# Kernel tuning notes

Hardware: AMD Instinct MI355X
Metric: run time of the kernel (lower is better)

The kernel has to match this reference:

```python
import jax, jax.numpy as jnp
import numpy as np

N_CLASSES = 80
N_ANCHORS = 3
ANCHORS = [[0.02403, 0.03125], [0.05469, 0.08221], [0.12109, 0.15104]]


def setup_inputs() -> dict:
    key = jax.random.key(0)
    B, W, H = 32, 76, 76
    C = (5 + N_CLASSES) * N_ANCHORS  # 255
    inputs = jax.random.normal(key, (B, C, W, H), dtype=jnp.float32)
    # anchors: [3,2] -> swapaxes -> [2,3] -> unsqueeze twice -> [2,1,1,3]
    anchors = jnp.asarray(ANCHORS, dtype=jnp.float32).swapaxes(0, 1).reshape(2, 1, 1, N_ANCHORS)
    return {"inputs": inputs, "anchors": anchors}


def reference(inputs, anchors):
    B, C, W, H = inputs.shape
    # split(85, dim=1) then cat on new last dim == reshape to [B,3,85,W,H] and
    # move the anchor-group axis to the end -> [B, 85, W, H, n_anchors]
    x = inputs.reshape(B, N_ANCHORS, 5 + N_CLASSES, W, H).transpose(0, 2, 3, 4, 1)
    t_xy = x[:, 0:2]            # [B,2,W,H,A]
    t_wh = x[:, 2:4]            # [B,2,W,H,A]
    objectness = x[:, 4:5]      # [B,1,W,H,A]
    class_prob = x[:, 5:]       # [B,80,W,H,A]

    # grid offsets: meshgrid 'ij' -> grid[0][i,j]=i, grid[1][i,j]=j
    gi, gj = jnp.meshgrid(jnp.arange(W), jnp.arange(H), indexing="ij")
    grid = jnp.stack([gi, gj], axis=0).reshape(1, 2, W, H, 1).astype(jnp.float32)
    n = jnp.asarray([W, H], dtype=jnp.float32).reshape(1, 2, 1, 1, 1)

    b_xy = (jax.nn.sigmoid(t_xy) + grid) / n          # [B,2,W,H,A]
    b_wh = jnp.exp(t_wh) * anchors                    # [B,2,W,H,A]

    conf = jax.nn.sigmoid(class_prob) * jax.nn.sigmoid(objectness)  # [B,80,W,H,A]
    conf = conf.reshape(B, N_CLASSES, -1).transpose(0, 2, 1)         # [B, W*H*A, 80]
    scores = jnp.max(conf, axis=2)                                   # [B, W*H*A]

    half = b_wh * 0.5
    x1y1 = b_xy - half
    x2y2 = b_xy + half
    boxes = jnp.concatenate([x1y1, x2y2], axis=1)     # [B,4,W,H,A]
    boxes = boxes.reshape(B, 4, -1).transpose(0, 2, 1)  # [B, W*H*A, 4]
    return boxes, conf, scores
```

## Files before the change

kernel.cpp:

```cpp
#include <hip/hip_runtime.h>


#define NCLS 80
#define NA   3
#define BB   32
#define WW   76
#define HH   76
#define WH   (WW*HH)
#define PP   (WH*NA)
#define TS   152
#define NT   38
#define CROW 84

typedef float f32x4 __attribute__((ext_vector_type(4)));

__global__ __launch_bounds__(512, 6) void yolo_conf_kernel(
    const float* __restrict__ in,
    float* __restrict__ conf,
    float* __restrict__ scores,
    float* __restrict__ scores_ws,
    int use_ws)
{
    __shared__ float cls[TS * CROW];
    __shared__ float so_arr[TS];

    const int t    = threadIdx.x;
    const int bid  = blockIdx.x;
    const int tile = bid % NT;
    const int ba   = bid / NT;
    const int a    = ba % NA;
    const int b    = ba / NA;
    const int s0   = tile * TS;

    const float* aplane = in + ((size_t)b * 255 + a * 85) * WH;

    if (t < TS)
        so_arr[t] = 1.0f / (1.0f + __expf(-aplane[(size_t)4 * WH + s0 + t]));

    #pragma unroll 3
    for (int it = 0; it < 6; ++it) {
        int u = it * 512 + t;
        if (u < 20 * TS) {
            int qq = u / TS;
            int sl = u - qq * TS;
            const float* gp = aplane + (size_t)(5 + qq * 4) * WH + s0 + sl;
            float v0 = gp[0];
            float v1 = gp[(size_t)1 * WH];
            float v2 = gp[(size_t)2 * WH];
            float v3 = gp[(size_t)3 * WH];
            *reinterpret_cast<float4*>(&cls[sl * CROW + qq * 4]) =
                make_float4(v0, v1, v2, v3);
        }
    }

    __syncthreads();

    size_t cbase = ((size_t)b * PP + (size_t)s0 * 3 + a) * NCLS;
    #pragma unroll 3
    for (int it = 0; it < 6; ++it) {
        int q = it * 512 + t;
        if (q < 20 * TS) {
            int sl = q / 20;
            int u  = q - sl * 20;
            float4 tv = *reinterpret_cast<const float4*>(&cls[sl * CROW + u * 4]);
            float so = so_arr[sl];
            f32x4 o;
            o.x = so / (1.0f + __expf(-tv.x));
            o.y = so / (1.0f + __expf(-tv.y));
            o.z = so / (1.0f + __expf(-tv.z));
            o.w = so / (1.0f + __expf(-tv.w));
            __builtin_nontemporal_store(o,
                reinterpret_cast<f32x4*>(conf + cbase + (size_t)sl * 240 + u * 4));
        }
    }

    if (t < TS) {
        float mx = -1e30f;
        #pragma unroll
        for (int u = 0; u < 20; ++u) {
            float4 v = *reinterpret_cast<const float4*>(&cls[t * CROW + u * 4]);
            mx = fmaxf(mx, fmaxf(fmaxf(v.x, v.y), fmaxf(v.z, v.w)));
        }
        float sc = so_arr[t] * (1.0f / (1.0f + __expf(-mx)));
        if (use_ws) {
            __builtin_nontemporal_store(sc,
                scores_ws + ((size_t)b * NA + a) * WH + s0 + t);
        } else {
            scores[(size_t)b * PP + (size_t)(s0 + t) * 3 + a] = sc;
        }
    }
}

__global__ __launch_bounds__(512, 4) void yolo_box_kernel(
    const float* __restrict__ in,
    const float* __restrict__ anchors,
    float* __restrict__ boxes,
    float* __restrict__ scores,
    const float* __restrict__ scores_ws,
    int use_ws)
{
    __shared__ float4 box_buf[TS * NA];
    __shared__ float  sc_buf[TS * NA];

    const int t    = threadIdx.x;
    const int bid  = blockIdx.x;
    const int tile = bid % NT;
    const int b    = bid / NT;
    const int s0   = tile * TS;

    if (t < TS * NA) {
        int aa = t / TS;
        int sl = t - aa * TS;
        int s  = s0 + sl;
        const float* hp = in + ((size_t)b * 255 + aa * 85) * WH + s;
        float tx = hp[0];
        float ty = hp[(size_t)1 * WH];
        float tw = hp[(size_t)2 * WH];
        float th = hp[(size_t)3 * WH];

        int w = s / HH, h = s - w * HH;
        float sx = 1.0f / (1.0f + __expf(-tx));
        float sy = 1.0f / (1.0f + __expf(-ty));
        float bx = (sx + (float)w) * (1.0f / WW);
        float by = (sy + (float)h) * (1.0f / HH);
        float bw = __expf(tw) * anchors[aa];
        float bh = __expf(th) * anchors[3 + aa];

        box_buf[sl * NA + aa] = make_float4(bx - 0.5f * bw, by - 0.5f * bh,
                                            bx + 0.5f * bw, by + 0.5f * bh);
        if (use_ws)
            sc_buf[sl * NA + aa] = scores_ws[((size_t)b * NA + aa) * WH + s];
    }

    __syncthreads();

    if (t < TS * NA) {
        float4 bq = box_buf[t];
        f32x4 bo = {bq.x, bq.y, bq.z, bq.w};
        __builtin_nontemporal_store(bo,
            reinterpret_cast<f32x4*>(boxes + ((size_t)b * PP + s0 * 3 + t) * 4));
        if (use_ws) {
            __builtin_nontemporal_store(sc_buf[t],
                scores + (size_t)b * PP + s0 * 3 + t);
        }
    }
}

extern "C" void kernel_launch(void* const* d_in, const int* in_sizes, int n_in,
                              void* d_out, int out_size, void* d_ws, size_t ws_size,
                              hipStream_t stream) {
    const float* in      = (const float*)d_in[0];
    const float* anchors = (const float*)d_in[1];

    float* boxes  = (float*)d_out;
    float* conf   = boxes + (size_t)BB * PP * 4;
    float* scores = conf + (size_t)BB * PP * NCLS;

    const size_t ws_need = (size_t)BB * NA * WH * sizeof(float);
    int use_ws = ws_size >= ws_need ? 1 : 0;
    float* scores_ws = (float*)d_ws;

    yolo_conf_kernel<<<BB * NA * NT, 512, 0, stream>>>(
        in, conf, scores, scores_ws, use_ws);
    yolo_box_kernel<<<BB * NT, 512, 0, stream>>>(
        in, anchors, boxes, scores, scores_ws, use_ws);
}
```

Measured before the change: 73.28 us.

## Fuse conf and box kernels into one decode kernel with XCD-aware block remap

Merges the two kernels into a single kernel in which each workgroup handles one 76-pixel tile across all three anchors. It computes boxes, objectness and per-anchor class confidences in one pass and writes scores directly, with no scores workspace round-trip. Block indices are remapped so consecutive tiles land on the same XCD, and the tile size is halved. This removes a kernel launch and the workspace traffic, at the cost of an anchor loop with two barriers per anchor and less parallelism per block.

```diff
diff --git a/kernel.cpp b/kernel.cpp
--- a/kernel.cpp
+++ b/kernel.cpp
@@ -8,141 +8,119 @@
 #define HH   76
 #define WH   (WW*HH)
 #define PP   (WH*NA)
-#define TS   152
-#define NT   38
+#define TS   76
+#define NTILE 76
 #define CROW 84
+#define NWG  (BB * NTILE)
+#define CPX  (NWG / 8)
 
 typedef float f32x4 __attribute__((ext_vector_type(4)));
 
-__global__ __launch_bounds__(512, 6) void yolo_conf_kernel(
-    const float* __restrict__ in,
-    float* __restrict__ conf,
-    float* __restrict__ scores,
-    float* __restrict__ scores_ws,
-    int use_ws)
-{
-    __shared__ float cls[TS * CROW];
-    __shared__ float so_arr[TS];
-
-    const int t    = threadIdx.x;
-    const int bid  = blockIdx.x;
-    const int tile = bid % NT;
-    const int ba   = bid / NT;
-    const int a    = ba % NA;
-    const int b    = ba / NA;
-    const int s0   = tile * TS;
-
-    const float* aplane = in + ((size_t)b * 255 + a * 85) * WH;
-
-    if (t < TS)
-        so_arr[t] = 1.0f / (1.0f + __expf(-aplane[(size_t)4 * WH + s0 + t]));
-
-    #pragma unroll 3
-    for (int it = 0; it < 6; ++it) {
-        int u = it * 512 + t;
-        if (u < 20 * TS) {
-            int qq = u / TS;
-            int sl = u - qq * TS;
-            const float* gp = aplane + (size_t)(5 + qq * 4) * WH + s0 + sl;
-            float v0 = gp[0];
-            float v1 = gp[(size_t)1 * WH];
-            float v2 = gp[(size_t)2 * WH];
-            float v3 = gp[(size_t)3 * WH];
-            *reinterpret_cast<float4*>(&cls[sl * CROW + qq * 4]) =
-                make_float4(v0, v1, v2, v3);
-        }
-    }
-
-    __syncthreads();
-
-    size_t cbase = ((size_t)b * PP + (size_t)s0 * 3 + a) * NCLS;
-    #pragma unroll 3
-    for (int it = 0; it < 6; ++it) {
-        int q = it * 512 + t;
-        if (q < 20 * TS) {
-            int sl = q / 20;
-            int u  = q - sl * 20;
-            float4 tv = *reinterpret_cast<const float4*>(&cls[sl * CROW + u * 4]);
-            float so = so_arr[sl];
-            f32x4 o;
-            o.x = so / (1.0f + __expf(-tv.x));
-            o.y = so / (1.0f + __expf(-tv.y));
-            o.z = so / (1.0f + __expf(-tv.z));
-            o.w = so / (1.0f + __expf(-tv.w));
-            __builtin_nontemporal_store(o,
-                reinterpret_cast<f32x4*>(conf + cbase + (size_t)sl * 240 + u * 4));
-        }
-    }
-
-    if (t < TS) {
-        float mx = -1e30f;
-        #pragma unroll
-        for (int u = 0; u < 20; ++u) {
-            float4 v = *reinterpret_cast<const float4*>(&cls[t * CROW + u * 4]);
-            mx = fmaxf(mx, fmaxf(fmaxf(v.x, v.y), fmaxf(v.z, v.w)));
-        }
-        float sc = so_arr[t] * (1.0f / (1.0f + __expf(-mx)));
-        if (use_ws) {
-            __builtin_nontemporal_store(sc,
-                scores_ws + ((size_t)b * NA + a) * WH + s0 + t);
-        } else {
-            scores[(size_t)b * PP + (size_t)(s0 + t) * 3 + a] = sc;
-        }
-    }
-}
-
-__global__ __launch_bounds__(512, 4) void yolo_box_kernel(
+__global__ __launch_bounds__(512, 8) void yolo_decode_kernel(
     const float* __restrict__ in,
     const float* __restrict__ anchors,
     float* __restrict__ boxes,
-    float* __restrict__ scores,
-    const float* __restrict__ scores_ws,
-    int use_ws)
+    float* __restrict__ conf,
+    float* __restrict__ scores)
 {
+    __shared__ float  cls[TS * CROW];
+    __shared__ float  so_buf[TS * NA];
+    __shared__ float  sc_buf[TS * NA];
     __shared__ float4 box_buf[TS * NA];
-    __shared__ float  sc_buf[TS * NA];
 
     const int t    = threadIdx.x;
-    const int bid  = blockIdx.x;
-    const int tile = bid % NT;
-    const int b    = bid / NT;
+    const int hw   = blockIdx.x;
+    const int bid  = (hw & 7) * CPX + (hw >> 3);
+    const int tile = bid % NTILE;
+    const int b    = bid / NTILE;
     const int s0   = tile * TS;
 
+    const float* bplane = in + (size_t)b * 255 * WH;
+
     if (t < TS * NA) {
-        int aa = t / TS;
-        int sl = t - aa * TS;
-        int s  = s0 + sl;
-        const float* hp = in + ((size_t)b * 255 + aa * 85) * WH + s;
+        int a_h  = t / TS;
+        int sl_h = t - a_h * TS;
+        const float* hp = bplane + (size_t)(a_h * 85) * WH + s0 + sl_h;
         float tx = hp[0];
         float ty = hp[(size_t)1 * WH];
         float tw = hp[(size_t)2 * WH];
         float th = hp[(size_t)3 * WH];
+        float to = hp[(size_t)4 * WH];
 
-        int w = s / HH, h = s - w * HH;
+        int s = s0 + sl_h;
+        int w = s / HH;
+        int h = s - w * HH;
         float sx = 1.0f / (1.0f + __expf(-tx));
         float sy = 1.0f / (1.0f + __expf(-ty));
         float bx = (sx + (float)w) * (1.0f / WW);
         float by = (sy + (float)h) * (1.0f / HH);
-        float bw = __expf(tw) * anchors[aa];
-        float bh = __expf(th) * anchors[3 + aa];
+        float bw = __expf(tw) * anchors[a_h];
+        float bh = __expf(th) * anchors[3 + a_h];
 
-        box_buf[sl * NA + aa] = make_float4(bx - 0.5f * bw, by - 0.5f * bh,
-                                            bx + 0.5f * bw, by + 0.5f * bh);
-        if (use_ws)
-            sc_buf[sl * NA + aa] = scores_ws[((size_t)b * NA + aa) * WH + s];
+        int p = sl_h * 3 + a_h;
+        box_buf[p] = make_float4(bx - 0.5f * bw, by - 0.5f * bh,
+                                 bx + 0.5f * bw, by + 0.5f * bh);
+        so_buf[p] = 1.0f / (1.0f + __expf(-to));
     }
 
-    __syncthreads();
+    for (int a = 0; a < NA; ++a) {
+        #pragma unroll
+        for (int it = 0; it < 3; ++it) {
+            int u = it * 512 + t;
+            if (u < 20 * TS) {
+                int qq = u / TS;
+                int sl = u - qq * TS;
+                const float* gp = bplane + (size_t)(a * 85 + 5 + qq * 4) * WH + s0 + sl;
+                float v0 = gp[0];
+                float v1 = gp[(size_t)1 * WH];
+                float v2 = gp[(size_t)2 * WH];
+                float v3 = gp[(size_t)3 * WH];
+                *reinterpret_cast<float4*>(&cls[sl * CROW + qq * 4]) =
+                    make_float4(v0, v1, v2, v3);
+            }
+        }
+
+        __syncthreads();
+
+        size_t cbase = ((size_t)b * PP + (size_t)s0 * 3 + a) * NCLS;
+        #pragma unroll
+        for (int it = 0; it < 3; ++it) {
+            int q = it * 512 + t;
+            if (q < 20 * TS) {
+                int sl = q / 20;
+                int u  = q - sl * 20;
+                float4 tv = *reinterpret_cast<const float4*>(&cls[sl * CROW + u * 4]);
+                float so = so_buf[sl * 3 + a];
+                f32x4 o;
+                o.x = so / (1.0f + __expf(-tv.x));
+                o.y = so / (1.0f + __expf(-tv.y));
+                o.z = so / (1.0f + __expf(-tv.z));
+                o.w = so / (1.0f + __expf(-tv.w));
+                __builtin_nontemporal_store(o,
+                    reinterpret_cast<f32x4*>(conf + cbase + (size_t)sl * 240 + u * 4));
+            }
+        }
+
+        if (t < TS) {
+            float mx = -1e30f;
+            #pragma unroll
+            for (int u = 0; u < 20; ++u) {
+                float4 v = *reinterpret_cast<const float4*>(&cls[t * CROW + u * 4]);
+                mx = fmaxf(mx, fmaxf(fmaxf(v.x, v.y), fmaxf(v.z, v.w)));
+            }
+            sc_buf[t * 3 + a] = so_buf[t * 3 + a] * (1.0f / (1.0f + __expf(-mx)));
+        }
+
+        __syncthreads();
+    }
 
     if (t < TS * NA) {
         float4 bq = box_buf[t];
         f32x4 bo = {bq.x, bq.y, bq.z, bq.w};
         __builtin_nontemporal_store(bo,
             reinterpret_cast<f32x4*>(boxes + ((size_t)b * PP + s0 * 3 + t) * 4));
-        if (use_ws) {
-            __builtin_nontemporal_store(sc_buf[t],
-                scores + (size_t)b * PP + s0 * 3 + t);
-        }
+        __builtin_nontemporal_store(sc_buf[t],
+            scores + (size_t)b * PP + s0 * 3 + t);
     }
 }
 
@@ -156,12 +134,5 @@
     float* conf   = boxes + (size_t)BB * PP * 4;
     float* scores = conf + (size_t)BB * PP * NCLS;
 
-    const size_t ws_need = (size_t)BB * NA * WH * sizeof(float);
-    int use_ws = ws_size >= ws_need ? 1 : 0;
-    float* scores_ws = (float*)d_ws;
-
-    yolo_conf_kernel<<<BB * NA * NT, 512, 0, stream>>>(
-        in, conf, scores, scores_ws, use_ws);
-    yolo_box_kernel<<<BB * NT, 512, 0, stream>>>(
-        in, anchors, boxes, scores, scores_ws, use_ws);
+    yolo_decode_kernel<<<NWG, 512, 0, stream>>>(in, anchors, boxes, conf, scores);
 }
```

Result: faster. 61.00 us (-16.8%).
